# Kernel tuning notes

Measured on AMD Instinct MI355X. Metric: run time of the kernel, lower is better.

Reference implementation:

```python
import jax, jax.numpy as jnp
import numpy as np

B, CN, DEG, IN_F, OUT_F, K = 32, 1024, 2, 128, 128, 10
NODES = [1, 16, 128, 1024]


def setup_inputs() -> dict:
    key = jax.random.key(0)
    ks = jax.random.split(key, 16)
    d = {}
    for i, n in enumerate(NODES):
        d[f"tree{i}"] = jax.random.normal(ks[i], (B, n, IN_F), dtype=jnp.float32)
    for i in range(4):
        d[f"Uw{i}"] = jax.random.normal(ks[4 + i], (IN_F, OUT_F), dtype=jnp.float32) * 0.05
        d[f"Ub{i}"] = jnp.zeros((OUT_F,), dtype=jnp.float32)
    d["W_up"] = jax.random.normal(ks[8], (CN, IN_F, DEG * IN_F), dtype=jnp.float32) * 0.05
    d["Fw0"] = jax.random.normal(ks[9], (IN_F, K * IN_F), dtype=jnp.float32) * 0.05
    d["Fb0"] = jnp.zeros((K * IN_F,), dtype=jnp.float32)
    d["Fw1"] = jax.random.normal(ks[10], (K * IN_F, OUT_F), dtype=jnp.float32) * 0.05
    d["Fb1"] = jnp.zeros((OUT_F,), dtype=jnp.float32)
    d["b_bias"] = jax.random.normal(ks[11], (1, DEG * CN, OUT_F), dtype=jnp.float32) * 0.05
    return d


def reference(tree0, tree1, tree2, tree3,
              Uw0, Ub0, Uw1, Ub1, Uw2, Ub2, Uw3, Ub3,
              W_up, Fw0, Fb0, Fw1, Fb1, b_bias):
    tree = [tree0, tree1, tree2, tree3]
    Uw = [Uw0, Uw1, Uw2, Uw3]
    Ub = [Ub0, Ub1, Ub2, Ub3]
    curr_node = W_up.shape[0]
    in_feat = W_up.shape[1]
    degree = W_up.shape[2] // in_feat

    # Ancestor info: project each depth, then tile each ancestor node's
    # projected vector to cover its descendants at the current level.
    anc = jnp.zeros((tree[0].shape[0], curr_node, Uw0.shape[1]), dtype=tree0.dtype)
    for t, w, b in zip(tree, Uw, Ub):
        Q = t @ w + b                       # [B, anc_node, out_feat]
        rep = curr_node // t.shape[1]
        anc = anc + jnp.repeat(Q, rep, axis=1)  # == tf.tile([1,1,rep]) + reshape

    # Per-node unique-weight upsample: [B,n,1,in] @ [n,in,deg*in]
    nl = jnp.einsum('bni,nio->bno', tree[-1], W_up)            # [B, CN, deg*in]
    nl = nl.reshape(nl.shape[0], curr_node * degree, in_feat)   # [B, CN*deg, in]
    nl = (nl @ Fw0 + Fb0) @ Fw1 + Fb1                           # Dense chain
    nl = nl + jnp.repeat(anc, degree, axis=1)                   # broadcast ancestors
    nl = nl + b_bias
    return jnp.where(nl >= 0, nl, 0.2 * nl)                     # LeakyReLU(0.2)
```

## Files before the change

### kernel.cpp

```cpp
#include <hip/hip_runtime.h>
#include <stdint.h>


using short8   = __attribute__((ext_vector_type(8))) short;
using floatx16 = __attribute__((ext_vector_type(16))) float;

__device__ __forceinline__ unsigned short f2bf(float f) {
    unsigned int u = __builtin_bit_cast(unsigned int, f);
    return (unsigned short)((u + 0x8000u) >> 16);
}

__device__ __forceinline__ short8 cvt8(const float* p) {
    const float4 v0 = *reinterpret_cast<const float4*>(p);
    const float4 v1 = *reinterpret_cast<const float4*>(p + 4);
    short8 a;
    a[0] = (short)f2bf(v0.x); a[1] = (short)f2bf(v0.y);
    a[2] = (short)f2bf(v0.z); a[3] = (short)f2bf(v0.w);
    a[4] = (short)f2bf(v1.x); a[5] = (short)f2bf(v1.y);
    a[6] = (short)f2bf(v1.z); a[7] = (short)f2bf(v1.w);
    return a;
}

__device__ __forceinline__ void gl_lds16(const float* g, float* l) {
    __builtin_amdgcn_global_load_lds(
        (const __attribute__((address_space(1))) unsigned int*)g,
        (__attribute__((address_space(3))) unsigned int*)l, 16, 0, 0);
}

#define P_FLOATS  264192
#define FB_OFF    264192
#define FF_OFF    264320
#define UW_OFF    272512

__global__ __launch_bounds__(256) void ffused_p1(
    const float* __restrict__ Fw0, const float* __restrict__ Fb0,
    const float* __restrict__ Fw1, float* __restrict__ P)
{
    const int kc = blockIdx.x;
    const int i  = blockIdx.y;
    const int j  = threadIdx.x & 127;
    const int il = threadIdx.x >> 7;
    const int k0 = kc * 160 + il * 80;
    const float* __restrict__ src = (i < 128) ? (Fw0 + (size_t)i * 1280) : Fb0;
    float acc = 0.f;
    #pragma unroll 8
    for (int kk = 0; kk < 80; ++kk)
        acc += src[k0 + kk] * Fw1[(size_t)(k0 + kk) * 128 + j];
    P[(size_t)(kc * 2 + il) * 16512 + i * 128 + j] = acc;
}

__global__ __launch_bounds__(256) void ffused_p2(
    const float* __restrict__ P, const float* __restrict__ Fb1,
    unsigned short* __restrict__ FfusedBF, float* __restrict__ Fbias)
{
    const int idx = blockIdx.x * 256 + threadIdx.x;
    if (idx >= 16512) return;
    const int i = idx >> 7, j = idx & 127;
    float s = 0.f;
    #pragma unroll
    for (int p = 0; p < 16; ++p) s += P[(size_t)p * 16512 + idx];
    if (i < 128) FfusedBF[(((i >> 3) * 128) + j) * 8 + (i & 7)] = f2bf(s);
    else         Fbias[j] = s + Fb1[j];
}

__global__ __launch_bounds__(256) void uwbf_kernel(
    const float* __restrict__ Uw0, const float* __restrict__ Uw1,
    const float* __restrict__ Uw2, const float* __restrict__ Uw3,
    unsigned short* __restrict__ UwBF)
{
    const int mat = blockIdx.x >> 4;
    const int kg  = blockIdx.x & 15;
    const float* __restrict__ Uw = (mat == 0) ? Uw0 : (mat == 1) ? Uw1
                                 : (mat == 2) ? Uw2 : Uw3;
    const int col = threadIdx.x & 127;
    const int kh  = threadIdx.x >> 7;
    #pragma unroll
    for (int q = 0; q < 4; ++q) {
        const int kk = kh * 4 + q;
        const float v = Uw[(size_t)(kg * 8 + kk) * 128 + col];
        UwBF[(((size_t)(mat * 16 + kg) * 128) + col) * 8 + kk] = f2bf(v);
    }
}

__global__ __launch_bounds__(256, 2) void tree_main(
    const float* __restrict__ t0, const float* __restrict__ t1,
    const float* __restrict__ t2, const float* __restrict__ t3,
    const float* __restrict__ Ub0, const float* __restrict__ Ub1,
    const float* __restrict__ Ub2, const float* __restrict__ Ub3,
    const float* __restrict__ Wup, const float* __restrict__ bbias,
    const unsigned short* __restrict__ FfusedBF,
    const unsigned short* __restrict__ UwBF,
    const float* __restrict__ Fbias,
    float* __restrict__ out)
{
    const int n    = blockIdx.x;
    const int tid  = threadIdx.x;
    const int w    = tid >> 6;
    const int lane = tid & 63;
    const int l31  = lane & 31;
    const int half = lane >> 5;
    const int colq = w * 32 + l31;

    __shared__ __align__(16) unsigned char smem_raw[16640];
    float*          Wlds = (float*)smem_raw;
    unsigned short* Ulds = (unsigned short*)smem_raw;

    floatx16 qacc;
    #pragma unroll
    for (int r = 0; r < 16; ++r) qacc[r] = 0.f;
    short8 af[8];
    const int b = l31;

    #pragma unroll
    for (int mi = 0; mi < 4; ++mi) {
        const float* base; int row;
        if      (mi == 0) { base = t0; row = b; }
        else if (mi == 1) { base = t1; row = b * 16 + (n >> 6); }
        else if (mi == 2) { base = t2; row = b * 128 + (n >> 3); }
        else              { base = t3; row = b * 1024 + n; }
        const float* rp = base + (size_t)row * 128;
        #pragma unroll
        for (int k8 = 0; k8 < 8; ++k8) {
            const short8 a = cvt8(rp + k8 * 16 + half * 8);
            const short8 bf = *reinterpret_cast<const short8*>(
                &UwBF[(((size_t)(mi * 16 + 2 * k8 + half) * 128) + colq) * 8]);
            qacc = __builtin_amdgcn_mfma_f32_32x32x16_bf16(a, bf, qacc, 0, 0, 0);
            if (mi == 3) af[k8] = a;
        }
    }

    floatx16 acc0, acc1;
    #pragma unroll
    for (int r = 0; r < 16; ++r) { acc0[r] = 0.f; acc1[r] = 0.f; }
    const float* Wn = Wup + (size_t)n * 32768;
    const int c0 = w * 64 + l31;
    #pragma unroll
    for (int ks = 0; ks < 8; ++ks) {
        __syncthreads();
        #pragma unroll
        for (int inst = 0; inst < 4; ++inst)
            gl_lds16(Wn + (size_t)ks * 4096 + inst * 1024 + tid * 4,
                     &Wlds[inst * 1024 + tid * 4]);
        __syncthreads();
        short8 b0, b1;
        #pragma unroll
        for (int jj = 0; jj < 8; ++jj) {
            const int krow = (half * 8 + jj) * 256;
            b0[jj] = (short)f2bf(Wlds[krow + c0]);
            b1[jj] = (short)f2bf(Wlds[krow + c0 + 32]);
        }
        acc0 = __builtin_amdgcn_mfma_f32_32x32x16_bf16(af[ks], b0, acc0, 0, 0, 0);
        acc1 = __builtin_amdgcn_mfma_f32_32x32x16_bf16(af[ks], b1, acc1, 0, 0, 0);
    }
    __syncthreads();

    #pragma unroll
    for (int tt = 0; tt < 2; ++tt) {
        const floatx16 Av = tt ? acc1 : acc0;
        const int c  = (2 * w + tt) * 32 + l31;
        const int d  = c >> 7;
        const int cp = c & 127;
        const unsigned off0 = (unsigned)((((cp >> 3) * 65) + d * 32) * 8 + (cp & 7));
        #pragma unroll
        for (int r = 0; r < 16; ++r) {
            const int brow = (r & 3) + 8 * (r >> 2) + 4 * half;
            Ulds[off0 + (unsigned)brow * 8] = f2bf(Av[r]);
        }
    }
    __syncthreads();

    floatx16 o0, o1;
    #pragma unroll
    for (int r = 0; r < 16; ++r) { o0[r] = 0.f; o1[r] = 0.f; }
    #pragma unroll
    for (int ks = 0; ks < 8; ++ks) {
        const int kg2 = 2 * ks + half;
        const short8 a0 = *reinterpret_cast<const short8*>(&Ulds[(kg2 * 65 + l31) * 8]);
        const short8 a1 = *reinterpret_cast<const short8*>(&Ulds[(kg2 * 65 + 32 + l31) * 8]);
        const short8 bf = *reinterpret_cast<const short8*>(
            &FfusedBF[(((size_t)kg2 * 128) + colq) * 8]);
        o0 = __builtin_amdgcn_mfma_f32_32x32x16_bf16(a0, bf, o0, 0, 0, 0);
        o1 = __builtin_amdgcn_mfma_f32_32x32x16_bf16(a1, bf, o1, 0, 0, 0);
    }

    const float ubsum = Ub0[colq] + Ub1[colq] + Ub2[colq] + Ub3[colq] + Fbias[colq];
    const float bb0 = bbias[(size_t)(2 * n + 0) * 128 + colq];
    const float bb1 = bbias[(size_t)(2 * n + 1) * 128 + colq];
    #pragma unroll
    for (int r = 0; r < 16; ++r) {
        const int brow = (r & 3) + 8 * (r >> 2) + 4 * half;
        const float addc = qacc[r] + ubsum;
        float v0 = o0[r] + addc + bb0;
        float v1 = o1[r] + addc + bb1;
        v0 = (v0 >= 0.f) ? v0 : 0.2f * v0;
        v1 = (v1 >= 0.f) ? v1 : 0.2f * v1;
        const size_t idx0 = ((size_t)brow * 2048 + 2 * n) * 128 + colq;
        out[idx0]       = v0;
        out[idx0 + 128] = v1;
    }
}

extern "C" void kernel_launch(void* const* d_in, const int* in_sizes, int n_in,
                              void* d_out, int out_size, void* d_ws, size_t ws_size,
                              hipStream_t stream) {
    const float* t0  = (const float*)d_in[0];
    const float* t1  = (const float*)d_in[1];
    const float* t2  = (const float*)d_in[2];
    const float* t3  = (const float*)d_in[3];
    const float* Uw0 = (const float*)d_in[4];
    const float* Ub0 = (const float*)d_in[5];
    const float* Uw1 = (const float*)d_in[6];
    const float* Ub1 = (const float*)d_in[7];
    const float* Uw2 = (const float*)d_in[8];
    const float* Ub2 = (const float*)d_in[9];
    const float* Uw3 = (const float*)d_in[10];
    const float* Ub3 = (const float*)d_in[11];
    const float* Wup = (const float*)d_in[12];
    const float* Fw0 = (const float*)d_in[13];
    const float* Fb0 = (const float*)d_in[14];
    const float* Fw1 = (const float*)d_in[15];
    const float* Fb1 = (const float*)d_in[16];
    const float* bb  = (const float*)d_in[17];

    float* ws = (float*)d_ws;
    float* P              = ws;
    float* Fbias          = ws + FB_OFF;
    unsigned short* FfBF  = (unsigned short*)(ws + FF_OFF);
    unsigned short* UwBF  = (unsigned short*)(ws + UW_OFF);

    ffused_p1<<<dim3(8, 129), 256, 0, stream>>>(Fw0, Fb0, Fw1, P);
    ffused_p2<<<65, 256, 0, stream>>>(P, Fb1, FfBF, Fbias);
    uwbf_kernel<<<64, 256, 0, stream>>>(Uw0, Uw1, Uw2, Uw3, UwBF);
    tree_main<<<1024, 256, 0, stream>>>(t0, t1, t2, t3,
                                        Ub0, Ub1, Ub2, Ub3,
                                        Wup, bb, FfBF, UwBF, Fbias,
                                        (float*)d_out);
}
```

Measured before the change: 297.7 us.

## Precompute ancestor projections separately and stream W_up via registers with transposed MFMA

Adds a qsum_kernel that computes the level-0..2 ancestor projections once per (batch, level-2 node) instead of recomputing them in each of the 1024 tree_main blocks. tree_main now stages t3 in LDS as bf16 and reads W_up straight from global into registers with one-step software prefetch, which removes the global_load_lds staging and its per-step barriers. The upsample MFMA is transposed so W_up supplies the A operand, and the LDS write-back layout is adjusted to match. This adds an extra launch and a Qsum global read per output element, and reuses workspace that the ffused kernels use as scratch.

```diff
diff --git a/kernel.cpp b/kernel.cpp
--- a/kernel.cpp
+++ b/kernel.cpp
@@ -21,16 +21,10 @@
     return a;
 }
 
-__device__ __forceinline__ void gl_lds16(const float* g, float* l) {
-    __builtin_amdgcn_global_load_lds(
-        (const __attribute__((address_space(1))) unsigned int*)g,
-        (__attribute__((address_space(3))) unsigned int*)l, 16, 0, 0);
-}
-
-#define P_FLOATS  264192
-#define FB_OFF    264192
-#define FF_OFF    264320
-#define UW_OFF    272512
+#define QS_OFF  0
+#define FB_OFF  524288
+#define FF_OFF  524416
+#define UW_OFF  532608
 
 __global__ __launch_bounds__(256) void ffused_p1(
     const float* __restrict__ Fw0, const float* __restrict__ Fb0,
@@ -82,15 +76,54 @@
     }
 }
 
+__global__ __launch_bounds__(256) void qsum_kernel(
+    const float* __restrict__ t0, const float* __restrict__ t1,
+    const float* __restrict__ t2, const unsigned short* __restrict__ UwBF,
+    float* __restrict__ Qsum)
+{
+    const int i2   = blockIdx.x;
+    const int tid  = threadIdx.x;
+    const int w    = tid >> 6;
+    const int lane = tid & 63;
+    const int l31  = lane & 31;
+    const int half = lane >> 5;
+    const int colq = w * 32 + l31;
+    const int b    = l31;
+
+    floatx16 acc;
+    #pragma unroll
+    for (int r = 0; r < 16; ++r) acc[r] = 0.f;
+
+    #pragma unroll
+    for (int mi = 0; mi < 3; ++mi) {
+        const float* base; int row;
+        if      (mi == 0) { base = t0; row = b; }
+        else if (mi == 1) { base = t1; row = b * 16 + (i2 >> 3); }
+        else              { base = t2; row = b * 128 + i2; }
+        const float* rp = base + (size_t)row * 128;
+        #pragma unroll
+        for (int k8 = 0; k8 < 8; ++k8) {
+            const short8 a  = cvt8(rp + k8 * 16 + half * 8);
+            const short8 bf = *reinterpret_cast<const short8*>(
+                &UwBF[(((size_t)(mi * 16 + 2 * k8 + half) * 128) + colq) * 8]);
+            acc = __builtin_amdgcn_mfma_f32_32x32x16_bf16(a, bf, acc, 0, 0, 0);
+        }
+    }
+    #pragma unroll
+    for (int r = 0; r < 16; ++r) {
+        const int brow = (r & 3) + 8 * (r >> 2) + 4 * half;
+        Qsum[((size_t)brow * 128 + i2) * 128 + colq] = acc[r];
+    }
+}
+
 __global__ __launch_bounds__(256, 2) void tree_main(
-    const float* __restrict__ t0, const float* __restrict__ t1,
-    const float* __restrict__ t2, const float* __restrict__ t3,
+    const float* __restrict__ t3,
     const float* __restrict__ Ub0, const float* __restrict__ Ub1,
     const float* __restrict__ Ub2, const float* __restrict__ Ub3,
     const float* __restrict__ Wup, const float* __restrict__ bbias,
     const unsigned short* __restrict__ FfusedBF,
     const unsigned short* __restrict__ UwBF,
-    const float* __restrict__ Fbias,
+    const float* __restrict__ Fbias, const float* __restrict__ Qsum,
     float* __restrict__ out)
 {
     const int n    = blockIdx.x;
@@ -102,69 +135,71 @@
     const int colq = w * 32 + l31;
 
     __shared__ __align__(16) unsigned char smem_raw[16640];
-    float*          Wlds = (float*)smem_raw;
-    unsigned short* Ulds = (unsigned short*)smem_raw;
-
-    floatx16 qacc;
-    #pragma unroll
-    for (int r = 0; r < 16; ++r) qacc[r] = 0.f;
-    short8 af[8];
-    const int b = l31;
-
-    #pragma unroll
-    for (int mi = 0; mi < 4; ++mi) {
-        const float* base; int row;
-        if      (mi == 0) { base = t0; row = b; }
-        else if (mi == 1) { base = t1; row = b * 16 + (n >> 6); }
-        else if (mi == 2) { base = t2; row = b * 128 + (n >> 3); }
-        else              { base = t3; row = b * 1024 + n; }
-        const float* rp = base + (size_t)row * 128;
-        #pragma unroll
-        for (int k8 = 0; k8 < 8; ++k8) {
-            const short8 a = cvt8(rp + k8 * 16 + half * 8);
-            const short8 bf = *reinterpret_cast<const short8*>(
-                &UwBF[(((size_t)(mi * 16 + 2 * k8 + half) * 128) + colq) * 8]);
-            qacc = __builtin_amdgcn_mfma_f32_32x32x16_bf16(a, bf, qacc, 0, 0, 0);
-            if (mi == 3) af[k8] = a;
-        }
-    }
-
-    floatx16 acc0, acc1;
-    #pragma unroll
-    for (int r = 0; r < 16; ++r) { acc0[r] = 0.f; acc1[r] = 0.f; }
-    const float* Wn = Wup + (size_t)n * 32768;
-    const int c0 = w * 64 + l31;
+    unsigned short* T3lds = (unsigned short*)smem_raw;
+    unsigned short* Ulds  = (unsigned short*)smem_raw;
+
+    #pragma unroll
+    for (int i = 0; i < 4; ++i) {
+        const int idx = i * 256 + tid;
+        const int b   = idx >> 5;
+        const int q   = idx & 31;
+        const float4 v = *reinterpret_cast<const float4*>(
+            t3 + ((size_t)b * 1024 + n) * 128 + q * 4);
+        ushort4 u;
+        u.x = f2bf(v.x); u.y = f2bf(v.y); u.z = f2bf(v.z); u.w = f2bf(v.w);
+        *reinterpret_cast<ushort4*>(&T3lds[((q >> 1) * 33 + b) * 8 + (q & 1) * 4]) = u;
+    }
+    __syncthreads();
+
+    floatx16 qacc, accT0, accT1;
+    #pragma unroll
+    for (int r = 0; r < 16; ++r) { qacc[r] = 0.f; accT0[r] = 0.f; accT1[r] = 0.f; }
+
+    const float* __restrict__ Wp0 = Wup + (size_t)n * 32768 + (half * 8) * 256 + w * 64 + l31;
+    const float* __restrict__ Wp1 = Wp0 + 32;
+
+    float p0[8], p1[8];
+    #pragma unroll
+    for (int jj = 0; jj < 8; ++jj) { p0[jj] = Wp0[jj * 256]; p1[jj] = Wp1[jj * 256]; }
+
     #pragma unroll
     for (int ks = 0; ks < 8; ++ks) {
-        __syncthreads();
-        #pragma unroll
-        for (int inst = 0; inst < 4; ++inst)
-            gl_lds16(Wn + (size_t)ks * 4096 + inst * 1024 + tid * 4,
-                     &Wlds[inst * 1024 + tid * 4]);
-        __syncthreads();
-        short8 b0, b1;
+        float n0[8], n1[8];
+        if (ks < 7) {
+            const int koff = (ks + 1) * 16 * 256;
+            #pragma unroll
+            for (int jj = 0; jj < 8; ++jj) {
+                n0[jj] = Wp0[koff + jj * 256];
+                n1[jj] = Wp1[koff + jj * 256];
+            }
+        }
+        const short8 afk = *reinterpret_cast<const short8*>(
+            &T3lds[((2 * ks + half) * 33 + l31) * 8]);
+        const short8 bfu = *reinterpret_cast<const short8*>(
+            &UwBF[(((size_t)(48 + 2 * ks + half) * 128) + colq) * 8]);
+        short8 a0, a1;
         #pragma unroll
         for (int jj = 0; jj < 8; ++jj) {
-            const int krow = (half * 8 + jj) * 256;
-            b0[jj] = (short)f2bf(Wlds[krow + c0]);
-            b1[jj] = (short)f2bf(Wlds[krow + c0 + 32]);
-        }
-        acc0 = __builtin_amdgcn_mfma_f32_32x32x16_bf16(af[ks], b0, acc0, 0, 0, 0);
-        acc1 = __builtin_amdgcn_mfma_f32_32x32x16_bf16(af[ks], b1, acc1, 0, 0, 0);
+            a0[jj] = (short)f2bf(p0[jj]);
+            a1[jj] = (short)f2bf(p1[jj]);
+        }
+        qacc  = __builtin_amdgcn_mfma_f32_32x32x16_bf16(afk, bfu, qacc, 0, 0, 0);
+        accT0 = __builtin_amdgcn_mfma_f32_32x32x16_bf16(a0, afk, accT0, 0, 0, 0);
+        accT1 = __builtin_amdgcn_mfma_f32_32x32x16_bf16(a1, afk, accT1, 0, 0, 0);
+        #pragma unroll
+        for (int jj = 0; jj < 8; ++jj) { p0[jj] = n0[jj]; p1[jj] = n1[jj]; }
     }
     __syncthreads();
 
     #pragma unroll
     for (int tt = 0; tt < 2; ++tt) {
-        const floatx16 Av = tt ? acc1 : acc0;
-        const int c  = (2 * w + tt) * 32 + l31;
-        const int d  = c >> 7;
-        const int cp = c & 127;
-        const unsigned off0 = (unsigned)((((cp >> 3) * 65) + d * 32) * 8 + (cp & 7));
+        const floatx16 Av = tt ? accT1 : accT0;
         #pragma unroll
         for (int r = 0; r < 16; ++r) {
-            const int brow = (r & 3) + 8 * (r >> 2) + 4 * half;
-            Ulds[off0 + (unsigned)brow * 8] = f2bf(Av[r]);
+            const int cm = w * 64 + tt * 32 + ((r & 3) + 8 * (r >> 2) + 4 * half);
+            const int d  = cm >> 7;
+            const int cp = cm & 127;
+            Ulds[(((cp >> 3) * 65) + d * 32 + l31) * 8 + (cp & 7)] = f2bf(Av[r]);
         }
     }
     __syncthreads();
@@ -186,10 +221,11 @@
     const float ubsum = Ub0[colq] + Ub1[colq] + Ub2[colq] + Ub3[colq] + Fbias[colq];
     const float bb0 = bbias[(size_t)(2 * n + 0) * 128 + colq];
     const float bb1 = bbias[(size_t)(2 * n + 1) * 128 + colq];
+    const int i2 = n >> 3;
     #pragma unroll
     for (int r = 0; r < 16; ++r) {
         const int brow = (r & 3) + 8 * (r >> 2) + 4 * half;
-        const float addc = qacc[r] + ubsum;
+        const float addc = qacc[r] + ubsum + Qsum[((size_t)brow * 128 + i2) * 128 + colq];
         float v0 = o0[r] + addc + bb0;
         float v1 = o1[r] + addc + bb1;
         v0 = (v0 >= 0.f) ? v0 : 0.2f * v0;
@@ -223,16 +259,17 @@
     const float* bb  = (const float*)d_in[17];
 
     float* ws = (float*)d_ws;
-    float* P              = ws;
+    float* Qsum           = ws + QS_OFF;
     float* Fbias          = ws + FB_OFF;
     unsigned short* FfBF  = (unsigned short*)(ws + FF_OFF);
     unsigned short* UwBF  = (unsigned short*)(ws + UW_OFF);
 
-    ffused_p1<<<dim3(8, 129), 256, 0, stream>>>(Fw0, Fb0, Fw1, P);
-    ffused_p2<<<65, 256, 0, stream>>>(P, Fb1, FfBF, Fbias);
+    ffused_p1<<<dim3(8, 129), 256, 0, stream>>>(Fw0, Fb0, Fw1, Qsum);
+    ffused_p2<<<65, 256, 0, stream>>>(Qsum, Fb1, FfBF, Fbias);
     uwbf_kernel<<<64, 256, 0, stream>>>(Uw0, Uw1, Uw2, Uw3, UwBF);
-    tree_main<<<1024, 256, 0, stream>>>(t0, t1, t2, t3,
+    qsum_kernel<<<128, 256, 0, stream>>>(t0, t1, t2, UwBF, Qsum);
+    tree_main<<<1024, 256, 0, stream>>>(t3,
                                         Ub0, Ub1, Ub2, Ub3,
-                                        Wup, bb, FfBF, UwBF, Fbias,
+                                        Wup, bb, FfBF, UwBF, Fbias, Qsum,
                                         (float*)d_out);
 }
```

Result: faster. 283.8 us (-4.7%).
